# Kernel optimization log

Hardware: AMD Instinct MI355X
Metric: run time of the kernel (lower is better)

The kernel has to match this reference:

```python
import jax, jax.numpy as jnp
import numpy as np

N_NODES = 100000
N_EDGES = 1600000
N_IN = 128
HID = 128
N_RATES = 16
EMB = 8
N_OUT = 2


def _lin_init(key, fan_in, fan_out):
    k1, k2 = jax.random.split(key)
    s = 1.0 / np.sqrt(fan_in)
    W = jax.random.uniform(k1, (fan_in, fan_out), jnp.float32, -s, s)
    b = jax.random.uniform(k2, (fan_out,), jnp.float32, -s, s)
    return W, b


def setup_inputs() -> dict:
    key = jax.random.key(0)
    ks = jax.random.split(key, 10)
    graph = jax.random.normal(ks[0], (N_NODES, N_IN), jnp.float32)
    edge_index = jax.random.randint(ks[1], (2, N_EDGES), 0, N_NODES, jnp.int64)
    rates = jax.random.normal(ks[2], (N_RATES,), jnp.float32)
    conv1_W, conv1_b = _lin_init(ks[3], N_IN, HID)
    enc_W1, enc_b1 = _lin_init(ks[4], N_RATES, EMB)
    enc_W2, enc_b2 = _lin_init(ks[5], EMB, HID)
    conv2_W, conv2_b = _lin_init(ks[6], 2 * HID, HID)
    conv3_W, conv3_b = _lin_init(ks[7], HID, HID)
    hid_W, hid_b = _lin_init(ks[8], HID, 2 * HID)
    k9a, k9b = jax.random.split(ks[9])
    hid2_W, hid2_b = _lin_init(k9a, 2 * HID, HID)
    fin_W, fin_b = _lin_init(k9b, HID, N_OUT)
    return dict(graph=graph, edge_index=edge_index, rates=rates,
                conv1_W=conv1_W, conv1_b=conv1_b,
                enc_W1=enc_W1, enc_b1=enc_b1, enc_W2=enc_W2, enc_b2=enc_b2,
                conv2_W=conv2_W, conv2_b=conv2_b,
                conv3_W=conv3_W, conv3_b=conv3_b,
                hid_W=hid_W, hid_b=hid_b, hid2_W=hid2_W, hid2_b=hid2_b,
                fin_W=fin_W, fin_b=fin_b)


def _gcn_conv(x, W, b, src, dst):
    # PyG GCNConv: x' = D^-1/2 (A + I) D^-1/2 (x W) + b, messages src->dst
    N = x.shape[0]
    h = x @ W  # [N, out]
    ones = jnp.ones(src.shape[0], h.dtype)
    deg = jax.ops.segment_sum(ones, dst, num_segments=N) + 1.0  # incl. self loop
    dinv = jax.lax.rsqrt(deg)  # [N]
    msg = h[src] * (dinv[src] * dinv[dst])[:, None]  # [E, out]
    agg = jax.ops.segment_sum(msg, dst, num_segments=N)
    return agg + h * (dinv * dinv)[:, None] + b  # self-loop term + bias


def reference(graph, edge_index, rates,
              conv1_W, conv1_b, enc_W1, enc_b1, enc_W2, enc_b2,
              conv2_W, conv2_b, conv3_W, conv3_b,
              hid_W, hid_b, hid2_W, hid2_b, fin_W, fin_b):
    src, dst = edge_index[0], edge_index[1]
    N = graph.shape[0]
    h = jax.nn.relu(_gcn_conv(graph, conv1_W, conv1_b, src, dst))
    # dropout is identity in eval mode
    r = jax.nn.relu(rates @ enc_W1 + enc_b1) @ enc_W2 + enc_b2  # [HID]
    h = jnp.concatenate([h, jnp.broadcast_to(r[None, :], (N, r.shape[0]))], axis=1)
    h = _gcn_conv(h, conv2_W, conv2_b, src, dst)
    h = _gcn_conv(h, conv3_W, conv3_b, src, dst)
    g = jnp.mean(h, axis=0, keepdims=True)  # global mean pool, batch=None -> [1, HID]
    g = jax.nn.relu(g @ hid_W + hid_b)
    g = jax.nn.relu(g @ hid2_W + hid2_b)
    return g @ fin_W + fin_b  # [1, N_OUT]
```

## Files before the change

kernel.cpp:

```cpp
#include <hip/hip_runtime.h>
#include <hip/hip_bf16.h>

#define HID 128

__global__ void count_deg_kernel(const int* __restrict__ dst, int* __restrict__ deg, int ne) {
    int e = blockIdx.x * blockDim.x + threadIdx.x;
    if (e < ne) atomicAdd(&deg[dst[e]], 1);
}

__global__ void scan_blocks_kernel(const int* __restrict__ deg, int* __restrict__ row_start,
                                   int* __restrict__ partials, int n) {
    __shared__ int sd[256];
    int t = threadIdx.x;
    int i = blockIdx.x * 256 + t;
    int v = (i < n) ? deg[i] : 0;
    sd[t] = v;
    __syncthreads();
    #pragma unroll
    for (int ofs = 1; ofs < 256; ofs <<= 1) {
        int x = (t >= ofs) ? sd[t - ofs] : 0;
        __syncthreads();
        sd[t] += x;
        __syncthreads();
    }
    if (i < n) row_start[i] = sd[t] - v;
    if (t == 255) partials[blockIdx.x] = sd[255];
}

__global__ void scan_partials_kernel(int* __restrict__ partials, int nb) {
    __shared__ int sd[512];
    int t = threadIdx.x;
    int v = (t < nb) ? partials[t] : 0;
    sd[t] = v;
    __syncthreads();
    #pragma unroll
    for (int ofs = 1; ofs < 512; ofs <<= 1) {
        int x = (t >= ofs) ? sd[t - ofs] : 0;
        __syncthreads();
        sd[t] += x;
        __syncthreads();
    }
    if (t < nb) partials[t] = sd[t] - v;
}

__global__ void scan_add_kernel(int* __restrict__ row_start, const int* __restrict__ partials, int n) {
    int i = blockIdx.x * 256 + threadIdx.x;
    if (i < n) row_start[i] += partials[blockIdx.x];
}

__global__ void dinv_kernel(const int* __restrict__ deg, float* __restrict__ dinv, int n) {
    int i = blockIdx.x * blockDim.x + threadIdx.x;
    if (i < n) dinv[i] = rsqrtf((float)deg[i] + 1.0f);
}

__global__ void fill_csr_kernel(const int* __restrict__ src, const int* __restrict__ dst,
                                const int* __restrict__ row_start, int* __restrict__ cursor,
                                int* __restrict__ csr_src, int ne) {
    int e = blockIdx.x * blockDim.x + threadIdx.x;
    if (e < ne) {
        int d = dst[e];
        int pos = atomicAdd(&cursor[d], 1);
        csr_src[row_start[d] + pos] = src[e];
    }
}

__global__ void rvec_kernel(const float* __restrict__ rates,
                            const float* __restrict__ eW1, const float* __restrict__ eb1,
                            const float* __restrict__ eW2, const float* __restrict__ eb2,
                            const float* __restrict__ conv2W, float* __restrict__ rb) {
    __shared__ float r1[8];
    __shared__ float rv[128];
    int f = threadIdx.x;
    if (f < 8) {
        float a = eb1[f];
        #pragma unroll
        for (int k = 0; k < 16; ++k) a += rates[k] * eW1[k * 8 + f];
        r1[f] = fmaxf(a, 0.f);
    }
    __syncthreads();
    float a = eb2[f];
    #pragma unroll
    for (int j = 0; j < 8; ++j) a += r1[j] * eW2[j * 128 + f];
    rv[f] = a;
    __syncthreads();
    float b = 0.f;
    for (int k = 0; k < 128; ++k) b += rv[k] * conv2W[(128 + k) * 128 + f];
    rb[f] = b;
}

#define FMA8(xs, wa, wb, A, B)                                          \
    A.x += (xs) * wa.x; A.y += (xs) * wa.y;                             \
    A.z += (xs) * wa.z; A.w += (xs) * wa.w;                             \
    B.x += (xs) * wb.x; B.y += (xs) * wb.y;                             \
    B.z += (xs) * wb.z; B.w += (xs) * wb.w;

#define KSTEP(KK, COMP)                                                 \
    {                                                                   \
        const float* wr = &wl[(k0 + KK) * 128 + col0];                  \
        float4 wa = *reinterpret_cast<const float4*>(wr);               \
        float4 wb = *reinterpret_cast<const float4*>(wr + 4);           \
        FMA8(xv0.COMP, wa, wb, a0a, a0b)                                \
        FMA8(xv1.COMP, wa, wb, a1a, a1b)                                \
        FMA8(xv2.COMP, wa, wb, a2a, a2b)                                \
        FMA8(xv3.COMP, wa, wb, a3a, a3b)                                \
    }

#define STORE_ROW(R, A, B)                                              \
    {                                                                   \
        int row = r0 + R;                                               \
        if (row < nrows) {                                              \
            const float dv = dinv[row];                                 \
            float4 o1, o2;                                              \
            o1.x = (A.x + ba.x) * dv; o1.y = (A.y + ba.y) * dv;         \
            o1.z = (A.z + ba.z) * dv; o1.w = (A.w + ba.w) * dv;         \
            o2.x = (B.x + bb.x) * dv; o2.y = (B.y + bb.y) * dv;         \
            o2.z = (B.z + bb.z) * dv; o2.w = (B.w + bb.w) * dv;         \
            float* op = out + (size_t)row * 128 + col0;                 \
            *reinterpret_cast<float4*>(op) = o1;                        \
            *reinterpret_cast<float4*>(op + 4) = o2;                    \
        }                                                               \
    }

__global__ __launch_bounds__(256) void gemm128_kernel(
    const float* __restrict__ X, const float* __restrict__ W,
    const float* __restrict__ bias, const float* __restrict__ dinv,
    float* __restrict__ out, int nrows) {
    __shared__ float wl[128 * 128];
    for (int i = threadIdx.x; i < 128 * 32; i += 256)
        reinterpret_cast<float4*>(wl)[i] = reinterpret_cast<const float4*>(W)[i];
    __syncthreads();

    const int t = threadIdx.x;
    const int cg = t & 15;
    const int rg = t >> 4;
    const int col0 = cg * 8;
    const int r0 = blockIdx.x * 64 + rg * 4;

    const float* x0 = X + (size_t)min(r0 + 0, nrows - 1) * 128;
    const float* x1 = X + (size_t)min(r0 + 1, nrows - 1) * 128;
    const float* x2 = X + (size_t)min(r0 + 2, nrows - 1) * 128;
    const float* x3 = X + (size_t)min(r0 + 3, nrows - 1) * 128;

    float4 a0a = {0,0,0,0}, a0b = {0,0,0,0};
    float4 a1a = {0,0,0,0}, a1b = {0,0,0,0};
    float4 a2a = {0,0,0,0}, a2b = {0,0,0,0};
    float4 a3a = {0,0,0,0}, a3b = {0,0,0,0};

    for (int k0 = 0; k0 < 128; k0 += 4) {
        float4 xv0 = *reinterpret_cast<const float4*>(x0 + k0);
        float4 xv1 = *reinterpret_cast<const float4*>(x1 + k0);
        float4 xv2 = *reinterpret_cast<const float4*>(x2 + k0);
        float4 xv3 = *reinterpret_cast<const float4*>(x3 + k0);
        KSTEP(0, x)
        KSTEP(1, y)
        KSTEP(2, z)
        KSTEP(3, w)
    }

    float4 ba = {0,0,0,0}, bb = {0,0,0,0};
    if (bias) {
        ba = *reinterpret_cast<const float4*>(bias + col0);
        bb = *reinterpret_cast<const float4*>(bias + col0 + 4);
    }
    STORE_ROW(0, a0a, a0b)
    STORE_ROW(1, a1a, a1b)
    STORE_ROW(2, a2a, a2b)
    STORE_ROW(3, a3a, a3b)
}

template <bool RELU, bool STORE, bool MEANPOOL>
__global__ __launch_bounds__(128) void agg_kernel(
    const float* __restrict__ hs, float* __restrict__ out,
    const float* __restrict__ dinv, const int* __restrict__ row_start,
    const int* __restrict__ csr_src, const float* __restrict__ bias,
    float* __restrict__ gsum, int n_nodes, int n_edges) {
    const int f = threadIdx.x;
    const float bf = bias[f];
    float msum = 0.f;
    for (int n = blockIdx.x; n < n_nodes; n += gridDim.x) {
        const int s = row_start[n];
        const int e = (n + 1 < n_nodes) ? row_start[n + 1] : n_edges;
        float acc0 = 0.f, acc1 = 0.f;
        int i = s;
        for (; i + 8 <= e; i += 8) {
            int s0 = csr_src[i + 0], s1 = csr_src[i + 1];
            int s2 = csr_src[i + 2], s3 = csr_src[i + 3];
            int s4 = csr_src[i + 4], s5 = csr_src[i + 5];
            int s6 = csr_src[i + 6], s7 = csr_src[i + 7];
            float h0 = hs[(size_t)s0 * 128 + f];
            float h1 = hs[(size_t)s1 * 128 + f];
            float h2 = hs[(size_t)s2 * 128 + f];
            float h3 = hs[(size_t)s3 * 128 + f];
            float h4 = hs[(size_t)s4 * 128 + f];
            float h5 = hs[(size_t)s5 * 128 + f];
            float h6 = hs[(size_t)s6 * 128 + f];
            float h7 = hs[(size_t)s7 * 128 + f];
            acc0 += (h0 + h1) + (h2 + h3);
            acc1 += (h4 + h5) + (h6 + h7);
        }
        for (; i < e; ++i) {
            int sI = csr_src[i];
            acc0 += hs[(size_t)sI * 128 + f];
        }
        const float di = dinv[n];
        float v = (acc0 + acc1 + hs[(size_t)n * 128 + f]) * di + bf;
        if (RELU) v = fmaxf(v, 0.f);
        if (STORE) out[(size_t)n * 128 + f] = v;
        if (MEANPOOL) msum += v;
    }
    if (MEANPOOL) atomicAdd(&gsum[f], msum);
}

__global__ void mlp_kernel(const float* __restrict__ gsum,
                           const float* __restrict__ hidW, const float* __restrict__ hidb,
                           const float* __restrict__ hid2W, const float* __restrict__ hid2b,
                           const float* __restrict__ finW, const float* __restrict__ finb,
                           float* __restrict__ out, float inv_n) {
    __shared__ float g[128], t1[256], t2[128];
    int t = threadIdx.x;
    if (t < 128) g[t] = gsum[t] * inv_n;
    __syncthreads();
    {
        float a = hidb[t];
        for (int k = 0; k < 128; ++k) a += g[k] * hidW[k * 256 + t];
        t1[t] = fmaxf(a, 0.f);
    }
    __syncthreads();
    if (t < 128) {
        float a = hid2b[t];
        for (int k = 0; k < 256; ++k) a += t1[k] * hid2W[k * 128 + t];
        t2[t] = fmaxf(a, 0.f);
    }
    __syncthreads();
    if (t < 2) {
        float a = finb[t];
        for (int k = 0; k < 128; ++k) a += t2[k] * finW[k * 2 + t];
        out[t] = a;
    }
}

extern "C" void kernel_launch(void* const* d_in, const int* in_sizes, int n_in,
                              void* d_out, int out_size, void* d_ws, size_t ws_size,
                              hipStream_t stream) {
    const float* graph  = (const float*)d_in[0];
    const int*   edge   = (const int*)d_in[1];
    const float* rates  = (const float*)d_in[2];
    const float* conv1W = (const float*)d_in[3];
    const float* conv1b = (const float*)d_in[4];
    const float* eW1    = (const float*)d_in[5];
    const float* eb1    = (const float*)d_in[6];
    const float* eW2    = (const float*)d_in[7];
    const float* eb2    = (const float*)d_in[8];
    const float* conv2W = (const float*)d_in[9];
    const float* conv2b = (const float*)d_in[10];
    const float* conv3W = (const float*)d_in[11];
    const float* conv3b = (const float*)d_in[12];
    const float* hidW   = (const float*)d_in[13];
    const float* hidb   = (const float*)d_in[14];
    const float* hid2W  = (const float*)d_in[15];
    const float* hid2b  = (const float*)d_in[16];
    const float* finW   = (const float*)d_in[17];
    const float* finb   = (const float*)d_in[18];

    const int NN = in_sizes[0] / 128;
    const int NE = in_sizes[1] / 2;
    const int* src = edge;
    const int* dst = edge + NE;

    char* ws = (char*)d_ws;
    size_t p = 0;
    auto alloc = [&](size_t bytes) { size_t o = p; p += (bytes + 511) & ~(size_t)511; return o; };
    int*   deg       = (int*)(ws + alloc((size_t)NN * 4));
    int*   cursor    = (int*)(ws + alloc((size_t)NN * 4));
    float* gsum      = (float*)(ws + alloc(512));
    const size_t zero_bytes = p;
    float* dinv      = (float*)(ws + alloc((size_t)NN * 4));
    int*   row_start = (int*)(ws + alloc((size_t)NN * 4));
    int*   partials  = (int*)(ws + alloc(512 * 4));
    int*   csr       = (int*)(ws + alloc((size_t)NE * 4));
    float* rb        = (float*)(ws + alloc(512));
    float* bufA      = (float*)(ws + alloc((size_t)NN * 128 * 4));
    float* bufB      = (float*)(ws + alloc((size_t)NN * 128 * 4));
    if (p > ws_size) return;

    const int SB = (NN + 255) / 256;
    const int EB = (NE + 255) / 256;

    hipMemsetAsync(d_ws, 0, zero_bytes, stream);
    count_deg_kernel<<<EB, 256, 0, stream>>>(dst, deg, NE);
    scan_blocks_kernel<<<SB, 256, 0, stream>>>(deg, row_start, partials, NN);
    scan_partials_kernel<<<1, 512, 0, stream>>>(partials, SB);
    scan_add_kernel<<<SB, 256, 0, stream>>>(row_start, partials, NN);
    dinv_kernel<<<(NN + 255) / 256, 256, 0, stream>>>(deg, dinv, NN);
    fill_csr_kernel<<<EB, 256, 0, stream>>>(src, dst, row_start, cursor, csr, NE);
    rvec_kernel<<<1, 128, 0, stream>>>(rates, eW1, eb1, eW2, eb2, conv2W, rb);

    const int GB = (NN + 63) / 64;

    gemm128_kernel<<<GB, 256, 0, stream>>>(graph, conv1W, nullptr, dinv, bufA, NN);
    agg_kernel<true, true, false><<<4096, 128, 0, stream>>>(bufA, bufB, dinv, row_start, csr, conv1b, nullptr, NN, NE);
    gemm128_kernel<<<GB, 256, 0, stream>>>(bufB, conv2W, rb, dinv, bufA, NN);
    agg_kernel<false, true, false><<<4096, 128, 0, stream>>>(bufA, bufB, dinv, row_start, csr, conv2b, nullptr, NN, NE);
    gemm128_kernel<<<GB, 256, 0, stream>>>(bufB, conv3W, nullptr, dinv, bufA, NN);
    agg_kernel<false, false, true><<<4096, 128, 0, stream>>>(bufA, nullptr, dinv, row_start, csr, conv3b, gsum, NN, NE);
    mlp_kernel<<<1, 256, 0, stream>>>(gsum, hidW, hidb, hid2W, hid2b, finW, finb, (float*)d_out, 1.0f / (float)NN);
}
```

Baseline: 960.7 us.

## Process four nodes per block with float4 vectorized gathers in aggregation

```diff
diff --git a/kernel.cpp b/kernel.cpp
--- a/kernel.cpp
+++ b/kernel.cpp
@@ -168,47 +168,69 @@
     STORE_ROW(3, a3a, a3b)
 }
 
+#define ACC4(A, H) A.x += H.x; A.y += H.y; A.z += H.z; A.w += H.w;
+
 template <bool RELU, bool STORE, bool MEANPOOL>
 __global__ __launch_bounds__(128) void agg_kernel(
     const float* __restrict__ hs, float* __restrict__ out,
     const float* __restrict__ dinv, const int* __restrict__ row_start,
     const int* __restrict__ csr_src, const float* __restrict__ bias,
     float* __restrict__ gsum, int n_nodes, int n_edges) {
-    const int f = threadIdx.x;
-    const float bf = bias[f];
-    float msum = 0.f;
-    for (int n = blockIdx.x; n < n_nodes; n += gridDim.x) {
-        const int s = row_start[n];
-        const int e = (n + 1 < n_nodes) ? row_start[n + 1] : n_edges;
-        float acc0 = 0.f, acc1 = 0.f;
-        int i = s;
-        for (; i + 8 <= e; i += 8) {
-            int s0 = csr_src[i + 0], s1 = csr_src[i + 1];
-            int s2 = csr_src[i + 2], s3 = csr_src[i + 3];
-            int s4 = csr_src[i + 4], s5 = csr_src[i + 5];
-            int s6 = csr_src[i + 6], s7 = csr_src[i + 7];
-            float h0 = hs[(size_t)s0 * 128 + f];
-            float h1 = hs[(size_t)s1 * 128 + f];
-            float h2 = hs[(size_t)s2 * 128 + f];
-            float h3 = hs[(size_t)s3 * 128 + f];
-            float h4 = hs[(size_t)s4 * 128 + f];
-            float h5 = hs[(size_t)s5 * 128 + f];
-            float h6 = hs[(size_t)s6 * 128 + f];
-            float h7 = hs[(size_t)s7 * 128 + f];
-            acc0 += (h0 + h1) + (h2 + h3);
-            acc1 += (h4 + h5) + (h6 + h7);
+    const int l = threadIdx.x & 31;
+    const int g = threadIdx.x >> 5;
+    const int f0 = l * 4;
+    const float4 bf = *reinterpret_cast<const float4*>(bias + f0);
+    float4 msum = {0, 0, 0, 0};
+    const int nq = (n_nodes + 3) >> 2;
+    for (int q = blockIdx.x; q < nq; q += gridDim.x) {
+        const int n = q * 4 + g;
+        if (n < n_nodes) {
+            const int s = row_start[n];
+            const int e = (n + 1 < n_nodes) ? row_start[n + 1] : n_edges;
+            float4 acc0 = {0,0,0,0}, acc1 = {0,0,0,0};
+            float4 acc2 = {0,0,0,0}, acc3 = {0,0,0,0};
+            int i = s;
+            for (; i + 4 <= e; i += 4) {
+                int s0 = csr_src[i + 0], s1 = csr_src[i + 1];
+                int s2 = csr_src[i + 2], s3 = csr_src[i + 3];
+                float4 h0 = *reinterpret_cast<const float4*>(hs + (size_t)s0 * 128 + f0);
+                float4 h1 = *reinterpret_cast<const float4*>(hs + (size_t)s1 * 128 + f0);
+                float4 h2 = *reinterpret_cast<const float4*>(hs + (size_t)s2 * 128 + f0);
+                float4 h3 = *reinterpret_cast<const float4*>(hs + (size_t)s3 * 128 + f0);
+                ACC4(acc0, h0) ACC4(acc1, h1) ACC4(acc2, h2) ACC4(acc3, h3)
+            }
+            for (; i < e; ++i) {
+                int sI = csr_src[i];
+                float4 hI = *reinterpret_cast<const float4*>(hs + (size_t)sI * 128 + f0);
+                ACC4(acc0, hI)
+            }
+            const float di = dinv[n];
+            const float4 self = *reinterpret_cast<const float4*>(hs + (size_t)n * 128 + f0);
+            float4 v;
+            v.x = (acc0.x + acc1.x + acc2.x + acc3.x + self.x) * di + bf.x;
+            v.y = (acc0.y + acc1.y + acc2.y + acc3.y + self.y) * di + bf.y;
+            v.z = (acc0.z + acc1.z + acc2.z + acc3.z + self.z) * di + bf.z;
+            v.w = (acc0.w + acc1.w + acc2.w + acc3.w + self.w) * di + bf.w;
+            if (RELU) {
+                v.x = fmaxf(v.x, 0.f); v.y = fmaxf(v.y, 0.f);
+                v.z = fmaxf(v.z, 0.f); v.w = fmaxf(v.w, 0.f);
+            }
+            if (STORE) *reinterpret_cast<float4*>(out + (size_t)n * 128 + f0) = v;
+            if (MEANPOOL) { ACC4(msum, v) }
         }
-        for (; i < e; ++i) {
-            int sI = csr_src[i];
-            acc0 += hs[(size_t)sI * 128 + f];
+    }
+    if (MEANPOOL) {
+        __shared__ float4 sred[4][32];
+        sred[g][l] = msum;
+        __syncthreads();
+        if (g == 0) {
+            float4 a = sred[0][l], b = sred[1][l], c = sred[2][l], d = sred[3][l];
+            atomicAdd(&gsum[f0 + 0], a.x + b.x + c.x + d.x);
+            atomicAdd(&gsum[f0 + 1], a.y + b.y + c.y + d.y);
+            atomicAdd(&gsum[f0 + 2], a.z + b.z + c.z + d.z);
+            atomicAdd(&gsum[f0 + 3], a.w + b.w + c.w + d.w);
         }
-        const float di = dinv[n];
-        float v = (acc0 + acc1 + hs[(size_t)n * 128 + f]) * di + bf;
-        if (RELU) v = fmaxf(v, 0.f);
-        if (STORE) out[(size_t)n * 128 + f] = v;
-        if (MEANPOOL) msum += v;
-    }
-    if (MEANPOOL) atomicAdd(&gsum[f], msum);
+    }
 }
 
 __global__ void mlp_kernel(const float* __restrict__ gsum,
```

Result: slower. 1.252 ms (+30.3%).

## Assign one wavefront per node with float2 loads in GCN aggregation

Applied to the files above, without the earlier changes.

```diff
diff --git a/kernel.cpp b/kernel.cpp
--- a/kernel.cpp
+++ b/kernel.cpp
@@ -168,47 +168,66 @@
     STORE_ROW(3, a3a, a3b)
 }
 
+#define ACC2(A, H) A.x += H.x; A.y += H.y;
+
 template <bool RELU, bool STORE, bool MEANPOOL>
-__global__ __launch_bounds__(128) void agg_kernel(
+__global__ __launch_bounds__(256) void agg_kernel(
     const float* __restrict__ hs, float* __restrict__ out,
     const float* __restrict__ dinv, const int* __restrict__ row_start,
     const int* __restrict__ csr_src, const float* __restrict__ bias,
     float* __restrict__ gsum, int n_nodes, int n_edges) {
-    const int f = threadIdx.x;
-    const float bf = bias[f];
-    float msum = 0.f;
-    for (int n = blockIdx.x; n < n_nodes; n += gridDim.x) {
+    const int l = threadIdx.x & 63;
+    const int w = threadIdx.x >> 6;
+    const int f0 = l * 2;
+    const float2 bf = *reinterpret_cast<const float2*>(bias + f0);
+    float2 msum = {0, 0};
+    const int stride = gridDim.x * 4;
+    for (int n = blockIdx.x * 4 + w; n < n_nodes; n += stride) {
         const int s = row_start[n];
         const int e = (n + 1 < n_nodes) ? row_start[n + 1] : n_edges;
-        float acc0 = 0.f, acc1 = 0.f;
+        float2 a0 = {0,0}, a1 = {0,0}, a2 = {0,0}, a3 = {0,0};
+        float2 a4 = {0,0}, a5 = {0,0}, a6 = {0,0}, a7 = {0,0};
         int i = s;
         for (; i + 8 <= e; i += 8) {
             int s0 = csr_src[i + 0], s1 = csr_src[i + 1];
             int s2 = csr_src[i + 2], s3 = csr_src[i + 3];
             int s4 = csr_src[i + 4], s5 = csr_src[i + 5];
             int s6 = csr_src[i + 6], s7 = csr_src[i + 7];
-            float h0 = hs[(size_t)s0 * 128 + f];
-            float h1 = hs[(size_t)s1 * 128 + f];
-            float h2 = hs[(size_t)s2 * 128 + f];
-            float h3 = hs[(size_t)s3 * 128 + f];
-            float h4 = hs[(size_t)s4 * 128 + f];
-            float h5 = hs[(size_t)s5 * 128 + f];
-            float h6 = hs[(size_t)s6 * 128 + f];
-            float h7 = hs[(size_t)s7 * 128 + f];
-            acc0 += (h0 + h1) + (h2 + h3);
-            acc1 += (h4 + h5) + (h6 + h7);
+            float2 h0 = *reinterpret_cast<const float2*>(hs + (size_t)s0 * 128 + f0);
+            float2 h1 = *reinterpret_cast<const float2*>(hs + (size_t)s1 * 128 + f0);
+            float2 h2 = *reinterpret_cast<const float2*>(hs + (size_t)s2 * 128 + f0);
+            float2 h3 = *reinterpret_cast<const float2*>(hs + (size_t)s3 * 128 + f0);
+            float2 h4 = *reinterpret_cast<const float2*>(hs + (size_t)s4 * 128 + f0);
+            float2 h5 = *reinterpret_cast<const float2*>(hs + (size_t)s5 * 128 + f0);
+            float2 h6 = *reinterpret_cast<const float2*>(hs + (size_t)s6 * 128 + f0);
+            float2 h7 = *reinterpret_cast<const float2*>(hs + (size_t)s7 * 128 + f0);
+            ACC2(a0, h0) ACC2(a1, h1) ACC2(a2, h2) ACC2(a3, h3)
+            ACC2(a4, h4) ACC2(a5, h5) ACC2(a6, h6) ACC2(a7, h7)
         }
         for (; i < e; ++i) {
             int sI = csr_src[i];
-            acc0 += hs[(size_t)sI * 128 + f];
+            float2 hI = *reinterpret_cast<const float2*>(hs + (size_t)sI * 128 + f0);
+            ACC2(a0, hI)
         }
         const float di = dinv[n];
-        float v = (acc0 + acc1 + hs[(size_t)n * 128 + f]) * di + bf;
-        if (RELU) v = fmaxf(v, 0.f);
-        if (STORE) out[(size_t)n * 128 + f] = v;
-        if (MEANPOOL) msum += v;
-    }
-    if (MEANPOOL) atomicAdd(&gsum[f], msum);
+        const float2 self = *reinterpret_cast<const float2*>(hs + (size_t)n * 128 + f0);
+        float2 v;
+        v.x = (((a0.x + a1.x) + (a2.x + a3.x)) + ((a4.x + a5.x) + (a6.x + a7.x)) + self.x) * di + bf.x;
+        v.y = (((a0.y + a1.y) + (a2.y + a3.y)) + ((a4.y + a5.y) + (a6.y + a7.y)) + self.y) * di + bf.y;
+        if (RELU) { v.x = fmaxf(v.x, 0.f); v.y = fmaxf(v.y, 0.f); }
+        if (STORE) *reinterpret_cast<float2*>(out + (size_t)n * 128 + f0) = v;
+        if (MEANPOOL) { ACC2(msum, v) }
+    }
+    if (MEANPOOL) {
+        __shared__ float2 sred[4][64];
+        sred[w][l] = msum;
+        __syncthreads();
+        if (w == 0) {
+            float2 a = sred[0][l], b = sred[1][l], c = sred[2][l], d = sred[3][l];
+            atomicAdd(&gsum[f0 + 0], (a.x + b.x) + (c.x + d.x));
+            atomicAdd(&gsum[f0 + 1], (a.y + b.y) + (c.y + d.y));
+        }
+    }
 }
 
 __global__ void mlp_kernel(const float* __restrict__ gsum,
@@ -296,12 +315,13 @@
     rvec_kernel<<<1, 128, 0, stream>>>(rates, eW1, eb1, eW2, eb2, conv2W, rb);
 
     const int GB = (NN + 63) / 64;
+    const int AB = 2048;
 
     gemm128_kernel<<<GB, 256, 0, stream>>>(graph, conv1W, nullptr, dinv, bufA, NN);
-    agg_kernel<true, true, false><<<4096, 128, 0, stream>>>(bufA, bufB, dinv, row_start, csr, conv1b, nullptr, NN, NE);
+    agg_kernel<true, true, false><<<AB, 256, 0, stream>>>(bufA, bufB, dinv, row_start, csr, conv1b, nullptr, NN, NE);
     gemm128_kernel<<<GB, 256, 0, stream>>>(bufB, conv2W, rb, dinv, bufA, NN);
-    agg_kernel<false, true, false><<<4096, 128, 0, stream>>>(bufA, bufB, dinv, row_start, csr, conv2b, nullptr, NN, NE);
+    agg_kernel<false, true, false><<<AB, 256, 0, stream>>>(bufA, bufB, dinv, row_start, csr, conv2b, nullptr, NN, NE);
     gemm128_kernel<<<GB, 256, 0, stream>>>(bufB, conv3W, nullptr, dinv, bufA, NN);
-    agg_kernel<false, false, true><<<4096, 128, 0, stream>>>(bufA, nullptr, dinv, row_start, csr, conv3b, gsum, NN, NE);
+    agg_kernel<false, false, true><<<AB, 256, 0, stream>>>(bufA, nullptr, dinv, row_start, csr, conv3b, gsum, NN, NE);
     mlp_kernel<<<1, 256, 0, stream>>>(gsum, hidW, hidb, hid2W, hid2b, finW, finb, (float*)d_out, 1.0f / (float)NN);
 }
```

Result: slower. 986.2 us (+2.6%).
